# Kernel optimization log

Hardware: AMD Instinct MI355X
Metric: run time of the kernel (lower is better)

The kernel has to match this reference:

```python
import jax, jax.numpy as jnp
import numpy as np

N_NODES = 100000
N_EDGES = 3200000


def gcn_conv(x, src, dst, W, b, n_nodes):
    """PyG-style GCNConv with self-loops and symmetric degree normalization.
    src/dst already include self-loops. Aggregates messages at dst."""
    deg = jax.ops.segment_sum(jnp.ones(dst.shape, dtype=x.dtype), dst,
                              num_segments=n_nodes)
    dinv = jnp.where(deg > 0, jax.lax.rsqrt(deg), 0.0)  # deg^{-1/2}
    xw = x @ W                                          # [N, out]
    norm = dinv[src] * dinv[dst]                        # [E]
    msg = xw[src] * norm[:, None]                       # gather + scale
    out = jax.ops.segment_sum(msg, dst, num_segments=n_nodes)
    return out + b


def setup_inputs() -> dict:
    key = jax.random.key(0)
    k1, k2, k3, k4 = jax.random.split(key, 4)
    x = jax.random.normal(k1, (N_NODES, 20), dtype=jnp.float32)
    edge_index = jax.random.randint(k2, (2, N_EDGES), 0, N_NODES, dtype=jnp.int64)
    # Glorot-ish init for weights
    W1 = jax.random.normal(k3, (20, 64), dtype=jnp.float32) * (1.0 / np.sqrt(20))
    b1 = jnp.zeros((64,), dtype=jnp.float32)
    W2 = jax.random.normal(k4, (64, 2), dtype=jnp.float32) * (1.0 / np.sqrt(64))
    b2 = jnp.zeros((2,), dtype=jnp.float32)
    return {"x": x, "edge_index": edge_index, "W1": W1, "b1": b1,
            "W2": W2, "b2": b2}


def reference(x, edge_index, W1, b1, W2, b2):
    n = x.shape[0]
    loops = jnp.arange(n, dtype=edge_index.dtype)
    src = jnp.concatenate([edge_index[0], loops])  # self-loops appended
    dst = jnp.concatenate([edge_index[1], loops])
    h = jax.nn.relu(gcn_conv(x, src, dst, W1, b1, n))
    out = gcn_conv(h, src, dst, W2, b2, n)
    return out
```

## Files before the change

kernel.cpp:

```cpp
#include <hip/hip_runtime.h>
#include <hip/hip_fp16.h>

#define F_IN 20
#define F_HID 64
#define F_OUT 2
#define BKT 256
#define MAXNB 512
#define STAGE_MAX 14336
#define G8 8
#define CHUNK 4096
#define PAD 16
#define CAP 10240
#define SPILLCAP 32768


__global__ void kinit(int* __restrict__ gcursor, int* __restrict__ spillcnt, int nb) {
    int i = blockIdx.x * blockDim.x + threadIdx.x;
    if (i < nb) gcursor[i * PAD] = i * CAP;
    if (i == 0) spillcnt[0] = 0;
}

__global__ __launch_bounds__(256) void kA2(const int* __restrict__ src,
                                           const int* __restrict__ dst,
                                           int* __restrict__ gcursor,
                                           int* __restrict__ bedge,
                                           int* __restrict__ spill,
                                           int* __restrict__ spillcnt,
                                           int e, int nb) {
    __shared__ unsigned short inv[CHUNK];
    __shared__ int cnt[MAXNB];
    __shared__ int lbase[MAXNB];
    __shared__ int lcur[MAXNB];
    __shared__ int gclaim[MAXNB];
    __shared__ int wtot[4];
    const int tid = threadIdx.x;
    const int lo = blockIdx.x * CHUNK;
    const int hi = min(e, lo + CHUNK);
    const int cn = hi - lo;
    for (int t = tid; t < MAXNB; t += 256) cnt[t] = 0;
    __syncthreads();
    for (int j = tid; j < cn; j += 256)
        atomicAdd(&cnt[dst[lo + j] >> 8], 1);
    __syncthreads();
    const int t2 = tid * 2;
    int v0 = cnt[t2], v1 = cnt[t2 + 1];
    int pv = v0 + v1;
    int sv = pv;
#pragma unroll
    for (int off = 1; off < 64; off <<= 1) {
        int u = __shfl_up(sv, off, 64);
        if ((tid & 63) >= off) sv += u;
    }
    if ((tid & 63) == 63) wtot[tid >> 6] = sv;
    __syncthreads();
    int wo = 0;
    for (int w = 0; w < (tid >> 6); ++w) wo += wtot[w];
    int excl = wo + sv - pv;
    lbase[t2] = excl;          lcur[t2] = excl;
    lbase[t2 + 1] = excl + v0; lcur[t2 + 1] = excl + v0;
    if (v0 && t2 < nb)     gclaim[t2]     = atomicAdd(&gcursor[t2 * PAD], v0);
    if (v1 && t2 + 1 < nb) gclaim[t2 + 1] = atomicAdd(&gcursor[(t2 + 1) * PAD], v1);
    __syncthreads();
    for (int j = tid; j < cn; j += 256) {
        int p = atomicAdd(&lcur[dst[lo + j] >> 8], 1);
        inv[p] = (unsigned short)j;
    }
    __syncthreads();
    for (int t = tid; t < cn; t += 256) {
        int j = inv[t];
        int d = dst[lo + j], s = src[lo + j];
        int b = d >> 8;
        int pos = gclaim[b] + (t - lbase[b]);
        if (pos < (b + 1) * CAP) {
            bedge[pos] = ((d & (BKT - 1)) << 20) | s;
        } else {
            int sp = atomicAdd(spillcnt, 1);
            if (sp < SPILLCAP) { spill[2 * sp] = d; spill[2 * sp + 1] = s; }
        }
    }
}

__global__ __launch_bounds__(256) void kB(int* __restrict__ bedge,
                                          const int* __restrict__ gcursor,
                                          int* __restrict__ row_ptr,
                                          int* __restrict__ rcnt,
                                          int* __restrict__ rdeg, int n) {
    __shared__ int stage[STAGE_MAX];
    __shared__ int hist[BKT];
    __shared__ int cur[BKT];
    __shared__ int wsum[4];
    const int tid = threadIdx.x, b = blockIdx.x;
    const int lo = b * CAP;
    int cnt = gcursor[b * PAD] - lo;
    if (cnt > CAP) cnt = CAP;
    hist[tid] = 0;
    __syncthreads();
    for (int j = tid; j < cnt; j += 256) {
        int w = bedge[lo + j];
        stage[j] = w;
        atomicAdd(&hist[((unsigned)w) >> 20], 1);
    }
    __syncthreads();
    int v = hist[tid];
    int sv = v;
#pragma unroll
    for (int off = 1; off < 64; off <<= 1) {
        int t = __shfl_up(sv, off, 64);
        if ((tid & 63) >= off) sv += t;
    }
    if ((tid & 63) == 63) wsum[tid >> 6] = sv;
    __syncthreads();
    int wo = 0;
    for (int w = 0; w < (tid >> 6); ++w) wo += wsum[w];
    int excl = wo + sv - v;
    cur[tid] = excl;
    int node = (b << 8) + tid;
    if (node < n) {
        row_ptr[node] = lo + excl;
        rcnt[node] = v;
        rdeg[node] = v;
    }
    __syncthreads();
    for (int j = tid; j < cnt; j += 256) {
        int w = stage[j];
        int pos = atomicAdd(&cur[((unsigned)w) >> 20], 1);
        bedge[lo + pos] = w & 1048575;
    }
}

__global__ void kFix(const int* __restrict__ spill, const int* __restrict__ spillcnt,
                     int* __restrict__ rdeg) {
    int m = spillcnt[0];
    if (m > SPILLCAP) m = SPILLCAP;
    int stride = gridDim.x * blockDim.x;
    for (int i = blockIdx.x * blockDim.x + threadIdx.x; i < m; i += stride)
        atomicAdd(&rdeg[spill[2 * i]], 1);
}

__global__ __launch_bounds__(256) void kxh_s(const float* __restrict__ x,
                                             const int* __restrict__ rdeg,
                                             unsigned* __restrict__ xhA,
                                             unsigned* __restrict__ xhB, int n) {
    int i = blockIdx.x * blockDim.x + threadIdx.x;
    if (i >= n) return;
    float dv = rsqrtf(1.0f + (float)rdeg[i]);
    const float4* xr = (const float4*)(x + (size_t)i * F_IN);
    unsigned w[10];
#pragma unroll
    for (int k = 0; k < 5; ++k) {
        float4 v = xr[k];
        __half2 h0 = __float22half2_rn(make_float2(v.x * dv, v.y * dv));
        __half2 h1 = __float22half2_rn(make_float2(v.z * dv, v.w * dv));
        w[k * 2 + 0] = *(const unsigned*)&h0;
        w[k * 2 + 1] = *(const unsigned*)&h1;
    }
    uint4* oa = (uint4*)(xhA + (size_t)i * 8);
    oa[0] = make_uint4(w[0], w[1], w[2], w[3]);
    oa[1] = make_uint4(w[4], w[5], w[6], w[7]);
    uint2* ob = (uint2*)(xhB + (size_t)i * 2);
    ob[0] = make_uint2(w[8], w[9]);
}

#define ACC2(u, idx) { float2 f_ = __half22float2(*(const __half2*)&(u)); \
                       acc[idx] += f_.x; acc[idx + 1] += f_.y; }

#define GATH1(s) { \
    const uint4* ra_ = (const uint4*)(xhA + (size_t)(s) * 8); \
    uint4 q0_ = ra_[0], q1_ = ra_[1]; \
    uint2 q2_ = *(const uint2*)(xhB + (size_t)(s) * 2); \
    ACC2(q0_.x, 0)  ACC2(q0_.y, 2)  ACC2(q0_.z, 4)  ACC2(q0_.w, 6) \
    ACC2(q1_.x, 8)  ACC2(q1_.y, 10) ACC2(q1_.z, 12) ACC2(q1_.w, 14) \
    ACC2(q2_.x, 16) ACC2(q2_.y, 18) }

__global__ __launch_bounds__(256) void kAgg_s(const int* __restrict__ bedge,
                                              const int* __restrict__ row_ptr,
                                              const int* __restrict__ rcnt,
                                              const int* __restrict__ rdeg,
                                              const int* __restrict__ spill,
                                              const int* __restrict__ spillcnt,
                                              const float* __restrict__ x,
                                              const unsigned* __restrict__ xhA,
                                              const unsigned* __restrict__ xhB,
                                              const float* __restrict__ W1,
                                              const float* __restrict__ b1,
                                              const float* __restrict__ W2,
                                              float* __restrict__ ts, int n) {
    __shared__ float W1s[F_IN * F_HID];
    __shared__ float b1s[F_HID];
    __shared__ float W2s[F_HID * F_OUT];
    for (int t = threadIdx.x; t < F_IN * F_HID; t += 256) W1s[t] = W1[t];
    if (threadIdx.x < F_HID) b1s[threadIdx.x] = b1[threadIdx.x];
    if (threadIdx.x < F_HID * F_OUT) W2s[threadIdx.x] = W2[threadIdx.x];
    __syncthreads();
    const int node = (blockIdx.x * 256 + threadIdx.x) >> 3;
    const int g = threadIdx.x & (G8 - 1);
    if (node >= n) return;
    const float dv = rsqrtf(1.0f + (float)rdeg[node]);
    float acc[F_IN];
#pragma unroll
    for (int k = 0; k < F_IN; ++k) acc[k] = 0.0f;
    {
        int jb = row_ptr[node], je = jb + rcnt[node];
        int j = jb + g;
        for (; j + G8 < je; j += 2 * G8) {
            int s0 = __builtin_nontemporal_load(&bedge[j]);
            int s1 = __builtin_nontemporal_load(&bedge[j + G8]);
            GATH1(s0)
            GATH1(s1)
        }
        if (j < je) {
            int s0 = __builtin_nontemporal_load(&bedge[j]);
            GATH1(s0)
        }
    }
    {
        int m = spillcnt[0];
        if (m > SPILLCAP) m = SPILLCAP;
        for (int i = g; i < m; i += G8) {
            if (spill[2 * i] == node) {
                int s0 = spill[2 * i + 1];
                GATH1(s0)
            }
        }
    }
    if (g == 0) {
        const float4* xr = (const float4*)(x + (size_t)node * F_IN);
#pragma unroll
        for (int k = 0; k < 5; ++k) {
            float4 vv = xr[k];
            acc[k * 4 + 0] = fmaf(vv.x, dv, acc[k * 4 + 0]);
            acc[k * 4 + 1] = fmaf(vv.y, dv, acc[k * 4 + 1]);
            acc[k * 4 + 2] = fmaf(vv.z, dv, acc[k * 4 + 2]);
            acc[k * 4 + 3] = fmaf(vv.w, dv, acc[k * 4 + 3]);
        }
    }
#pragma unroll
    for (int k = 0; k < F_IN; ++k) {
        acc[k] += __shfl_xor(acc[k], 1, 64);
        acc[k] += __shfl_xor(acc[k], 2, 64);
        acc[k] += __shfl_xor(acc[k], 4, 64);
        acc[k] *= dv;
    }
    float t0 = 0.0f, t1 = 0.0f;
#pragma unroll
    for (int jj = 0; jj < 8; ++jj) {
        int j = g * 8 + jj;
        float a = b1s[j];
#pragma unroll
        for (int k = 0; k < F_IN; ++k) a = fmaf(acc[k], W1s[k * F_HID + j], a);
        float h = fmaxf(a, 0.0f);
        t0 = fmaf(h, W2s[j * F_OUT + 0], t0);
        t1 = fmaf(h, W2s[j * F_OUT + 1], t1);
    }
    t0 += __shfl_xor(t0, 1, 64); t0 += __shfl_xor(t0, 2, 64); t0 += __shfl_xor(t0, 4, 64);
    t1 += __shfl_xor(t1, 1, 64); t1 += __shfl_xor(t1, 2, 64); t1 += __shfl_xor(t1, 4, 64);
    if (g == 0) *(float2*)(ts + (size_t)node * 2) = make_float2(t0 * dv, t1 * dv);
}

__global__ __launch_bounds__(256) void kL2g(const int* __restrict__ bedge,
                                            const int* __restrict__ row_ptr,
                                            const int* __restrict__ rcnt,
                                            const int* __restrict__ rdeg,
                                            const int* __restrict__ spill,
                                            const int* __restrict__ spillcnt,
                                            const float* __restrict__ ts,
                                            const float* __restrict__ b2,
                                            float* __restrict__ out, int n) {
    const int node = (blockIdx.x * 256 + threadIdx.x) >> 3;
    const int g = threadIdx.x & (G8 - 1);
    if (node >= n) return;
    float a0 = 0.0f, a1 = 0.0f;
    {
        int jb = row_ptr[node], je = jb + rcnt[node];
        int j = jb + g;
        for (; j + G8 < je; j += 2 * G8) {
            int s0 = __builtin_nontemporal_load(&bedge[j]);
            int s1 = __builtin_nontemporal_load(&bedge[j + G8]);
            float2 u0 = *(const float2*)(ts + (size_t)s0 * 2);
            float2 u1 = *(const float2*)(ts + (size_t)s1 * 2);
            a0 += u0.x + u1.x; a1 += u0.y + u1.y;
        }
        if (j < je) {
            int s0 = __builtin_nontemporal_load(&bedge[j]);
            float2 u0 = *(const float2*)(ts + (size_t)s0 * 2);
            a0 += u0.x; a1 += u0.y;
        }
    }
    {
        int m = spillcnt[0];
        if (m > SPILLCAP) m = SPILLCAP;
        for (int i = g; i < m; i += G8) {
            if (spill[2 * i] == node) {
                float2 u = *(const float2*)(ts + (size_t)spill[2 * i + 1] * 2);
                a0 += u.x; a1 += u.y;
            }
        }
    }
    a0 += __shfl_xor(a0, 1, 64); a0 += __shfl_xor(a0, 2, 64); a0 += __shfl_xor(a0, 4, 64);
    a1 += __shfl_xor(a1, 1, 64); a1 += __shfl_xor(a1, 2, 64); a1 += __shfl_xor(a1, 4, 64);
    if (g == 0) {
        float dv = rsqrtf(1.0f + (float)rdeg[node]);
        float2 t = *(const float2*)(ts + (size_t)node * 2);
        *(float2*)(out + (size_t)node * 2) =
            make_float2(b2[0] + (a0 + t.x) * dv, b2[1] + (a1 + t.y) * dv);
    }
}


__global__ void k_zero_i(int* __restrict__ p, int n) {
    int i = blockIdx.x * blockDim.x + threadIdx.x;
    if (i < n) p[i] = 0;
}
__global__ void k_hist(const int* __restrict__ dst, int* __restrict__ counts, int e) {
    int i = blockIdx.x * blockDim.x + threadIdx.x;
    if (i < e) atomicAdd(&counts[dst[i]], 1);
}
__global__ __launch_bounds__(1024) void k_scan(const int* __restrict__ counts,
                                               int* __restrict__ row_ptr,
                                               int* __restrict__ cursor, int n) {
    __shared__ int warp_sums[16];
    __shared__ int carry_s;
    const int tid = threadIdx.x;
    const int lane = tid & 63, wid = tid >> 6;
    if (tid == 0) carry_s = 0;
    __syncthreads();
    for (int base = 0; base < n; base += 1024) {
        int i = base + tid;
        int v = (i < n) ? counts[i] : 0;
        int sv = v;
#pragma unroll
        for (int off = 1; off < 64; off <<= 1) {
            int t = __shfl_up(sv, off, 64);
            if (lane >= off) sv += t;
        }
        if (lane == 63) warp_sums[wid] = sv;
        __syncthreads();
        if (wid == 0 && lane < 16) {
            int ws = warp_sums[lane];
#pragma unroll
            for (int off = 1; off < 16; off <<= 1) {
                int t = __shfl_up(ws, off, 16);
                if (lane >= off) ws += t;
            }
            warp_sums[lane] = ws;
        }
        __syncthreads();
        int wofs = (wid > 0) ? warp_sums[wid - 1] : 0;
        int excl = carry_s + wofs + sv - v;
        if (i < n) { row_ptr[i] = excl; cursor[i] = excl; }
        __syncthreads();
        if (tid == 0) carry_s += warp_sums[15];
        __syncthreads();
    }
    if (tid == 0) row_ptr[n] = carry_s;
}
__global__ void k_fill(const int* __restrict__ src, const int* __restrict__ dst,
                       int* __restrict__ cursor, int* __restrict__ edge_src, int e) {
    int i = blockIdx.x * blockDim.x + threadIdx.x;
    if (i >= e) return;
    int s = src[i], d = dst[i];
    int pos = atomicAdd(&cursor[d], 1);
    edge_src[pos] = s;
}
__global__ void k_dinv_fb(const int* __restrict__ counts, float* __restrict__ dinv, int n) {
    int i = blockIdx.x * blockDim.x + threadIdx.x;
    if (i < n) dinv[i] = rsqrtf(1.0f + (float)counts[i]);
}
__global__ void k_gather_mlp(const int* __restrict__ row_ptr, const int* __restrict__ edge_src,
                             const float* __restrict__ x, const float* __restrict__ dinv,
                             const float* __restrict__ W1, const float* __restrict__ b1,
                             const float* __restrict__ W2, float* __restrict__ ts, int n) {
    __shared__ float W1s[F_IN * F_HID];
    __shared__ float b1s[F_HID];
    __shared__ float W2s[F_HID * F_OUT];
    for (int t = threadIdx.x; t < F_IN * F_HID; t += blockDim.x) W1s[t] = W1[t];
    if (threadIdx.x < F_HID) b1s[threadIdx.x] = b1[threadIdx.x];
    if (threadIdx.x < F_HID * F_OUT) W2s[threadIdx.x] = W2[threadIdx.x];
    __syncthreads();
    int i = blockIdx.x * blockDim.x + threadIdx.x;
    if (i >= n) return;
    float dv = dinv[i];
    float acc[F_IN];
    {
        float d2 = dv * dv;
        const float4* xr = (const float4*)(x + (size_t)i * F_IN);
#pragma unroll
        for (int k = 0; k < 5; ++k) {
            float4 v = xr[k];
            acc[k * 4 + 0] = v.x * d2; acc[k * 4 + 1] = v.y * d2;
            acc[k * 4 + 2] = v.z * d2; acc[k * 4 + 3] = v.w * d2;
        }
    }
    int jb = row_ptr[i], je = row_ptr[i + 1];
    for (int j = jb; j < je; ++j) {
        int s = edge_src[j];
        float w = dinv[s] * dv;
        const float4* xr = (const float4*)(x + (size_t)s * F_IN);
#pragma unroll
        for (int k = 0; k < 5; ++k) {
            float4 v = xr[k];
            acc[k * 4 + 0] = fmaf(v.x, w, acc[k * 4 + 0]);
            acc[k * 4 + 1] = fmaf(v.y, w, acc[k * 4 + 1]);
            acc[k * 4 + 2] = fmaf(v.z, w, acc[k * 4 + 2]);
            acc[k * 4 + 3] = fmaf(v.w, w, acc[k * 4 + 3]);
        }
    }
    float t0 = 0.0f, t1 = 0.0f;
#pragma unroll 8
    for (int j = 0; j < F_HID; ++j) {
        float a = b1s[j];
#pragma unroll
        for (int k = 0; k < F_IN; ++k) a = fmaf(acc[k], W1s[k * F_HID + j], a);
        float h = fmaxf(a, 0.0f);
        t0 = fmaf(h, W2s[j * F_OUT + 0], t0);
        t1 = fmaf(h, W2s[j * F_OUT + 1], t1);
    }
    ts[(size_t)i * 2 + 0] = t0 * dv;
    ts[(size_t)i * 2 + 1] = t1 * dv;
}
__global__ void k_gather2(const int* __restrict__ row_ptr, const int* __restrict__ edge_src,
                          const float* __restrict__ ts, const float* __restrict__ dinv,
                          const float* __restrict__ b2, float* __restrict__ out, int n) {
    int i = blockIdx.x * blockDim.x + threadIdx.x;
    if (i >= n) return;
    float dv = dinv[i];
    float2 t = *(const float2*)(ts + (size_t)i * 2);
    float a0 = t.x, a1 = t.y;
    int jb = row_ptr[i], je = row_ptr[i + 1];
    for (int j = jb; j < je; ++j) {
        int s = edge_src[j];
        float2 v = *(const float2*)(ts + (size_t)s * 2);
        a0 += v.x; a1 += v.y;
    }
    out[(size_t)i * 2 + 0] = b2[0] + a0 * dv;
    out[(size_t)i * 2 + 1] = b2[1] + a1 * dv;
}


extern "C" void kernel_launch(void* const* d_in, const int* in_sizes, int n_in,
                              void* d_out, int out_size, void* d_ws, size_t ws_size,
                              hipStream_t stream) {
    const float* x  = (const float*)d_in[0];
    const int*   ei = (const int*)d_in[1];
    const float* W1 = (const float*)d_in[2];
    const float* b1 = (const float*)d_in[3];
    const float* W2 = (const float*)d_in[4];
    const float* b2 = (const float*)d_in[5];
    float* out = (float*)d_out;

    const int n = in_sizes[0] / F_IN;
    const int e = in_sizes[1] / 2;
    const int* src = ei;
    const int* dst = ei + e;

    const int B = 256;
    const int gn = (n + B - 1) / B;
    const int ge = (e + B - 1) / B;

    const int NB = (n + BKT - 1) / BKT;
    size_t base_words = (size_t)NB * PAD + PAD + 2 * (size_t)SPILLCAP
                      + (size_t)NB * CAP + 5 * (size_t)n;
    size_t xh_off_words = (base_words + 3) & ~(size_t)3;
    size_t need_cap = xh_off_words * 4 + (size_t)n * 40;
    bool cap_ok = ((size_t)NB * CAP >= (size_t)e + NB) && (CAP <= STAGE_MAX);

    if (n < (1 << 20) && NB <= MAXNB && cap_ok && ws_size >= need_cap) {
        int*   gcursor  = (int*)d_ws;
        int*   spillcnt = gcursor + (size_t)NB * PAD;
        int*   spill    = spillcnt + PAD;
        int*   bedge    = spill + 2 * (size_t)SPILLCAP;
        int*   row_ptr  = bedge + (size_t)NB * CAP;
        int*   rcnt     = row_ptr + n;
        int*   rdeg     = rcnt + n;
        float* ts       = (float*)(rdeg + n);
        unsigned* xhA   = (unsigned*)((int*)d_ws + xh_off_words);
        unsigned* xhB   = xhA + (size_t)n * 8;

        kinit<<<(NB + 255) / 256, 256, 0, stream>>>(gcursor, spillcnt, NB);
        kA2<<<(e + CHUNK - 1) / CHUNK, 256, 0, stream>>>(src, dst, gcursor, bedge,
                                                         spill, spillcnt, e, NB);
        kB<<<NB, 256, 0, stream>>>(bedge, gcursor, row_ptr, rcnt, rdeg, n);
        kFix<<<16, 256, 0, stream>>>(spill, spillcnt, rdeg);
        kxh_s<<<gn, B, 0, stream>>>(x, rdeg, xhA, xhB, n);
        int gg8 = ((size_t)n * G8 + 255) / 256;
        kAgg_s<<<gg8, 256, 0, stream>>>(bedge, row_ptr, rcnt, rdeg, spill, spillcnt,
                                        x, xhA, xhB, W1, b1, W2, ts, n);
        kL2g<<<gg8, 256, 0, stream>>>(bedge, row_ptr, rcnt, rdeg, spill, spillcnt,
                                      ts, b2, out, n);
    } else {
        int*   counts   = (int*)d_ws;
        int*   row_ptr  = counts + n;
        int*   cursor   = row_ptr + n + 1;
        int*   edge_src = cursor + n;
        float* dinv     = (float*)(edge_src + e);
        float* ts       = dinv + n;

        k_zero_i<<<gn, B, 0, stream>>>(counts, n);
        k_hist<<<ge, B, 0, stream>>>(dst, counts, e);
        k_scan<<<1, 1024, 0, stream>>>(counts, row_ptr, cursor, n);
        k_fill<<<ge, B, 0, stream>>>(src, dst, cursor, edge_src, e);
        k_dinv_fb<<<gn, B, 0, stream>>>(counts, dinv, n);
        k_gather_mlp<<<gn, B, 0, stream>>>(row_ptr, edge_src, x, dinv, W1, b1, W2, ts, n);
        k_gather2<<<gn, B, 0, stream>>>(row_ptr, edge_src, ts, dinv, b2, out, n);
    }
}
```

Before: 173.2 us.

## Simplify edge bucketing to direct LDS-atomic placement with smaller chunks

The bucketing kernel drops the local prefix scan and the shared-memory inverse permutation that wrote edges out in bucket-sorted order. Each edge now takes its global slot directly from an LDS atomic on a per-bucket cursor seeded from the global claim. The chunk size is halved so more blocks run, and the kB stage buffer is shrunk. This removes two barriers, the scan and an LDS pass, but global writes become less coalesced and the global cursor atomics double because there are twice as many blocks.

```diff
diff --git a/kernel.cpp b/kernel.cpp
--- a/kernel.cpp
+++ b/kernel.cpp
@@ -6,9 +6,9 @@
 #define F_OUT 2
 #define BKT 256
 #define MAXNB 512
-#define STAGE_MAX 14336
+#define STAGE_MAX 10240
 #define G8 8
-#define CHUNK 4096
+#define CHUNK 2048
 #define PAD 16
 #define CAP 10240
 #define SPILLCAP 32768
@@ -27,50 +27,25 @@
                                            int* __restrict__ spill,
                                            int* __restrict__ spillcnt,
                                            int e, int nb) {
-    __shared__ unsigned short inv[CHUNK];
     __shared__ int cnt[MAXNB];
-    __shared__ int lbase[MAXNB];
     __shared__ int lcur[MAXNB];
-    __shared__ int gclaim[MAXNB];
-    __shared__ int wtot[4];
     const int tid = threadIdx.x;
     const int lo = blockIdx.x * CHUNK;
     const int hi = min(e, lo + CHUNK);
-    const int cn = hi - lo;
     for (int t = tid; t < MAXNB; t += 256) cnt[t] = 0;
     __syncthreads();
-    for (int j = tid; j < cn; j += 256)
-        atomicAdd(&cnt[dst[lo + j] >> 8], 1);
-    __syncthreads();
-    const int t2 = tid * 2;
-    int v0 = cnt[t2], v1 = cnt[t2 + 1];
-    int pv = v0 + v1;
-    int sv = pv;
-#pragma unroll
-    for (int off = 1; off < 64; off <<= 1) {
-        int u = __shfl_up(sv, off, 64);
-        if ((tid & 63) >= off) sv += u;
-    }
-    if ((tid & 63) == 63) wtot[tid >> 6] = sv;
-    __syncthreads();
-    int wo = 0;
-    for (int w = 0; w < (tid >> 6); ++w) wo += wtot[w];
-    int excl = wo + sv - pv;
-    lbase[t2] = excl;          lcur[t2] = excl;
-    lbase[t2 + 1] = excl + v0; lcur[t2 + 1] = excl + v0;
-    if (v0 && t2 < nb)     gclaim[t2]     = atomicAdd(&gcursor[t2 * PAD], v0);
-    if (v1 && t2 + 1 < nb) gclaim[t2 + 1] = atomicAdd(&gcursor[(t2 + 1) * PAD], v1);
-    __syncthreads();
-    for (int j = tid; j < cn; j += 256) {
-        int p = atomicAdd(&lcur[dst[lo + j] >> 8], 1);
-        inv[p] = (unsigned short)j;
-    }
-    __syncthreads();
-    for (int t = tid; t < cn; t += 256) {
-        int j = inv[t];
-        int d = dst[lo + j], s = src[lo + j];
+    for (int j = lo + tid; j < hi; j += 256)
+        atomicAdd(&cnt[dst[j] >> 8], 1);
+    __syncthreads();
+    for (int t = tid; t < nb; t += 256) {
+        int c = cnt[t];
+        if (c) lcur[t] = atomicAdd(&gcursor[t * PAD], c);
+    }
+    __syncthreads();
+    for (int j = lo + tid; j < hi; j += 256) {
+        int d = dst[j], s = src[j];
         int b = d >> 8;
-        int pos = gclaim[b] + (t - lbase[b]);
+        int pos = atomicAdd(&lcur[b], 1);
         if (pos < (b + 1) * CAP) {
             bedge[pos] = ((d & (BKT - 1)) << 20) | s;
         } else {
```

Result: slower. 200.4 us (+15.7%).
